# Kernel optimization log

Measured on AMD Instinct MI355X. Metric: run time of the kernel, lower is better.

## Reference

```python
import jax, jax.numpy as jnp
import numpy as np

N = 100000
NFEAT = 128
NHID = 16
HEADS = 8
NCLASS = 40
E = 1600000
NEG_SLOPE = 0.2  # PyG GATConv default


def glorot(key, shape):
    fan = shape[0] + shape[-1]
    limit = float(np.sqrt(6.0 / fan))
    return jax.random.uniform(key, shape, jnp.float32, -limit, limit)


def setup_inputs() -> dict:
    key = jax.random.key(0)
    ks = jax.random.split(key, 10)
    x = jax.random.normal(ks[0], (N, NFEAT), jnp.float32)
    adj = jnp.zeros((1,), jnp.float32)  # unused by forward, kept for signature parity
    edge_index = jax.random.randint(ks[1], (2, E), 0, N, jnp.int64)
    # layer 1: GATConv(NFEAT, NHID, heads=HEADS)
    W1 = glorot(ks[2], (NFEAT, HEADS * NHID))
    att_src1 = glorot(ks[3], (HEADS, NHID))
    att_dst1 = glorot(ks[4], (HEADS, NHID))
    b1 = jnp.zeros((HEADS * NHID,), jnp.float32)
    # layer 2: GATConv(HEADS*NHID, NCLASS, heads=1)
    W2 = glorot(ks[5], (HEADS * NHID, NCLASS))
    att_src2 = glorot(ks[6], (1, NCLASS))
    att_dst2 = glorot(ks[7], (1, NCLASS))
    b2 = jnp.zeros((NCLASS,), jnp.float32)
    return {"x": x, "adj": adj, "edge_index": edge_index,
            "W1": W1, "att_src1": att_src1, "att_dst1": att_dst1, "b1": b1,
            "W2": W2, "att_src2": att_src2, "att_dst2": att_dst2, "b2": b2}


def gat_conv(x, W, att_src, att_dst, bias, src, dst, heads, out_ch):
    n = x.shape[0]
    h = (x @ W).reshape(n, heads, out_ch)              # [N,H,C]
    a_src = (h * att_src[None]).sum(-1)                # [N,H]
    a_dst = (h * att_dst[None]).sum(-1)                # [N,H]
    e = jax.nn.leaky_relu(a_src[src] + a_dst[dst], NEG_SLOPE)  # [E,H]
    # softmax over incoming edges of each destination node
    m = jax.ops.segment_max(e, dst, num_segments=n)
    e = jnp.exp(e - m[dst])
    s = jax.ops.segment_sum(e, dst, num_segments=n)
    alpha = e / s[dst]                                  # [E,H]
    msg = h[src] * alpha[:, :, None]                    # [E,H,C]
    out = jax.ops.segment_sum(msg, dst, num_segments=n)  # [N,H,C]
    return out.reshape(n, heads * out_ch) + bias


def reference(x, adj, edge_index, W1, att_src1, att_dst1, b1, W2, att_src2, att_dst2, b2):
    # PyG GATConv adds self-loops by default
    loops = jnp.arange(N, dtype=edge_index.dtype)
    src = jnp.concatenate([edge_index[0], loops])
    dst = jnp.concatenate([edge_index[1], loops])
    # eval mode: F.dropout is identity
    h = jax.nn.elu(gat_conv(x, W1, att_src1, att_dst1, b1, src, dst, HEADS, NHID))
    h = jax.nn.elu(gat_conv(h, W2, att_src2, att_dst2, b2, src, dst, 1, NCLASS))
    return jax.nn.log_softmax(h, axis=1)
```

## Files before the change

kernel.cpp:

```cpp
#include <hip/hip_runtime.h>
#include <stdint.h>

#define NEG_SLOPE 0.2f

__device__ __forceinline__ float lrelu(float v) { return v >= 0.f ? v : NEG_SLOPE * v; }
__device__ __forceinline__ float elu(float v) { return v > 0.f ? v : expm1f(v); }
__device__ __forceinline__ float pexp(float v) { return __expf(lrelu(v)); }

typedef _Float16 h16x2 __attribute__((ext_vector_type(2)));
typedef _Float16 half8 __attribute__((ext_vector_type(8)));
typedef float floatx4 __attribute__((ext_vector_type(4)));

__device__ __forceinline__ void fma_h2(float& a0, float& a1, float p, unsigned u) {
    h16x2 h = __builtin_bit_cast(h16x2, u);
    a0 += p * (float)h[0];
    a1 += p * (float)h[1];
}


__global__ void prep_kernel(const float* __restrict__ W1, const float* __restrict__ W2,
                            _Float16* __restrict__ w1t, _Float16* __restrict__ w2t,
                            int* __restrict__ deg, int n) {
    int t = blockIdx.x * 256 + threadIdx.x;
    if (t < n) deg[t] = 0;
    if (t < 128 * 128) {
        int col = t >> 7, k = t & 127;
        w1t[col * 128 + k] = (_Float16)W1[k * 128 + col];
    }
    if (t < 48 * 128) {
        int col = t >> 7, k = t & 127;
        w2t[t] = (col < 40) ? (_Float16)W2[k * 40 + col] : (_Float16)0.f;
    }
}


__global__ void hist_kernel(const int* __restrict__ ei, int* __restrict__ deg,
                            unsigned* __restrict__ rankd, int E, int n) {
    int e = blockIdx.x * blockDim.x + threadIdx.x;
    if (e >= E) return;
    int d = ei[E + e];
    unsigned rd = 0xFFFFFFFFu;
    if ((unsigned)d < (unsigned)n)
        rd = ((unsigned)d << 7) | (unsigned)atomicAdd(&deg[d], 1);
    rankd[e] = rd;
}

#define SCAN_T 256
#define SCAN_TILE 1024

__global__ __launch_bounds__(SCAN_T) void scan_p1_kernel(const int* __restrict__ deg,
                                                         int* __restrict__ bsum, int n) {
    __shared__ int red[SCAN_T];
    int t = threadIdx.x;
    int base = blockIdx.x * SCAN_TILE + t * 4;
    int s = 0;
    #pragma unroll
    for (int i = 0; i < 4; i++) {
        int idx = base + i;
        if (idx < n) s += deg[idx];
    }
    red[t] = s;
    __syncthreads();
    for (int off = SCAN_T / 2; off; off >>= 1) {
        if (t < off) red[t] += red[t + off];
        __syncthreads();
    }
    if (t == 0) bsum[blockIdx.x] = red[0];
}

__global__ __launch_bounds__(SCAN_T) void scan_p3f_kernel(const int* __restrict__ deg,
                                                          const int* __restrict__ bsum,
                                                          int* __restrict__ row_ptr,
                                                          int n, int nbk) {
    __shared__ int red[SCAN_T];
    int t = threadIdx.x;
    red[t] = (t < nbk && t < blockIdx.x) ? bsum[t] : 0;
    __syncthreads();
    for (int off = SCAN_T / 2; off; off >>= 1) {
        if (t < off) red[t] += red[t + off];
        __syncthreads();
    }
    const int blockoff = red[0];
    __syncthreads();

    int base = blockIdx.x * SCAN_TILE + t * 4;
    int v[4];
    int s = 0;
    #pragma unroll
    for (int i = 0; i < 4; i++) {
        int idx = base + i;
        v[i] = (idx < n) ? deg[idx] : 0;
        s += v[i];
    }
    red[t] = s;
    __syncthreads();
    for (int off = 1; off < SCAN_T; off <<= 1) {
        int add = (t >= off) ? red[t - off] : 0;
        __syncthreads();
        red[t] += add;
        __syncthreads();
    }
    int excl = red[t] - s + blockoff;
    #pragma unroll
    for (int i = 0; i < 4; i++) {
        int idx = base + i;
        if (idx < n) row_ptr[idx] = excl;
        excl += v[i];
        if (idx == n - 1) row_ptr[n] = excl;
    }
}

__global__ void scatter_kernel(const int* __restrict__ ei, const unsigned* __restrict__ rankd,
                               const int* __restrict__ row_ptr,
                               int* __restrict__ csr_src, int E) {
    int e = blockIdx.x * blockDim.x + threadIdx.x;
    if (e >= E) return;
    unsigned rd = rankd[e];
    if (rd == 0xFFFFFFFFu) return;
    csr_src[row_ptr[rd >> 7] + (int)(rd & 127u)] = ei[e];
}


__global__ __launch_bounds__(256) void gemm1_mfma_kernel(
    const float* __restrict__ x, const _Float16* __restrict__ w1t,
    const float* __restrict__ as1, const float* __restrict__ ad1,
    _Float16* __restrict__ h1h, float* __restrict__ a1s, float* __restrict__ a1d, int n) {
    __shared__ __align__(16) char Wl[32768];
    const int tid = threadIdx.x;
    {
        const uint4* Wg = (const uint4*)w1t;
        #pragma unroll
        for (int i = 0; i < 8; i++) {
            int it = tid + i * 256;
            uint4 v = Wg[it];
            int b = it * 16;
            *(uint4*)&Wl[b ^ (((b >> 8) & 7) << 4)] = v;
        }
    }
    const int wave = tid >> 6, lane = tid & 63;
    const int cl = lane & 15, g = lane >> 4;
    const int wbase = blockIdx.x * 64 + wave * 16;

    int arow = wbase + cl;
    if (arow >= n) arow = n - 1;
    half8 afr[4];
    #pragma unroll
    for (int t = 0; t < 4; t++) {
        const float4 v0 = *(const float4*)&x[(size_t)arow * 128 + 32 * t + g * 8];
        const float4 v1 = *(const float4*)&x[(size_t)arow * 128 + 32 * t + g * 8 + 4];
        afr[t][0] = (_Float16)v0.x; afr[t][1] = (_Float16)v0.y;
        afr[t][2] = (_Float16)v0.z; afr[t][3] = (_Float16)v0.w;
        afr[t][4] = (_Float16)v1.x; afr[t][5] = (_Float16)v1.y;
        afr[t][6] = (_Float16)v1.z; afr[t][7] = (_Float16)v1.w;
    }
    __syncthreads();

    #pragma unroll
    for (int ct = 0; ct < 8; ct++) {
        const int col = ct * 16 + cl;
        half8 bfr[4];
        #pragma unroll
        for (int t = 0; t < 4; t++) {
            int b = (col << 8) + 64 * t + 16 * g;
            bfr[t] = *(half8*)&Wl[b ^ ((col & 7) << 4)];
        }
        floatx4 acc = {0.f, 0.f, 0.f, 0.f};
        #pragma unroll
        for (int t = 0; t < 4; t++)
            acc = __builtin_amdgcn_mfma_f32_16x16x32_f16(afr[t], bfr[t], acc, 0, 0, 0);
        const float av = as1[col], dv = ad1[col];
        #pragma unroll
        for (int i = 0; i < 4; i++) {
            int r = wbase + g * 4 + i;
            float hv = acc[i];
            if (r < n) h1h[(size_t)r * 128 + col] = (_Float16)hv;
            float ps = hv * av, pd = hv * dv;
            ps += __shfl_xor(ps, 1); ps += __shfl_xor(ps, 2);
            ps += __shfl_xor(ps, 4); ps += __shfl_xor(ps, 8);
            pd += __shfl_xor(pd, 1); pd += __shfl_xor(pd, 2);
            pd += __shfl_xor(pd, 4); pd += __shfl_xor(pd, 8);
            if (cl == 0 && r < n) {
                a1s[r * 8 + ct] = ps;
                a1d[r * 8 + ct] = pd;
            }
        }
    }
}

__global__ __launch_bounds__(256) void agg1_kernel(const int* __restrict__ row_ptr,
                                                   const int* __restrict__ csr_src,
                                                   const float* __restrict__ a1s,
                                                   const float* __restrict__ a1d,
                                                   const uint4* __restrict__ h1q,
                                                   const float* __restrict__ b1,
                                                   _Float16* __restrict__ h2h, int n) {
    int lane = threadIdx.x & 63;
    int d = blockIdx.x * 4 + (threadIdx.x >> 6);
    if (d >= n) return;
    const int g = lane >> 4;
    const int q = lane & 15;
    const int h = q >> 1;
    const float adh = a1d[d * 8 + h];

    float acc[8];
    #pragma unroll
    for (int i = 0; i < 8; i++) acc[i] = 0.f;
    float sum = 0.f;
    if (g == 0) {
        uint4 w = h1q[(size_t)d * 16 + q];
        float ps = pexp(a1s[d * 8 + h] + adh);
        fma_h2(acc[0], acc[1], ps, w.x);
        fma_h2(acc[2], acc[3], ps, w.y);
        fma_h2(acc[4], acc[5], ps, w.z);
        fma_h2(acc[6], acc[7], ps, w.w);
        sum = ps;
    }
    int beg = row_ptr[d], end = row_ptr[d + 1];
    int e = beg + g;
    for (; e + 12 < end; e += 16) {
        int s0 = csr_src[e],     s1 = csr_src[e + 4];
        int s2 = csr_src[e + 8], s3 = csr_src[e + 12];
        uint4 w0 = h1q[(size_t)s0 * 16 + q];
        uint4 w1 = h1q[(size_t)s1 * 16 + q];
        uint4 w2 = h1q[(size_t)s2 * 16 + q];
        uint4 w3 = h1q[(size_t)s3 * 16 + q];
        float p0 = pexp(a1s[s0 * 8 + h] + adh);
        float p1 = pexp(a1s[s1 * 8 + h] + adh);
        float p2 = pexp(a1s[s2 * 8 + h] + adh);
        float p3 = pexp(a1s[s3 * 8 + h] + adh);
        fma_h2(acc[0], acc[1], p0, w0.x); fma_h2(acc[2], acc[3], p0, w0.y);
        fma_h2(acc[4], acc[5], p0, w0.z); fma_h2(acc[6], acc[7], p0, w0.w);
        fma_h2(acc[0], acc[1], p1, w1.x); fma_h2(acc[2], acc[3], p1, w1.y);
        fma_h2(acc[4], acc[5], p1, w1.z); fma_h2(acc[6], acc[7], p1, w1.w);
        fma_h2(acc[0], acc[1], p2, w2.x); fma_h2(acc[2], acc[3], p2, w2.y);
        fma_h2(acc[4], acc[5], p2, w2.z); fma_h2(acc[6], acc[7], p2, w2.w);
        fma_h2(acc[0], acc[1], p3, w3.x); fma_h2(acc[2], acc[3], p3, w3.y);
        fma_h2(acc[4], acc[5], p3, w3.z); fma_h2(acc[6], acc[7], p3, w3.w);
        sum += (p0 + p1) + (p2 + p3);
    }
    for (; e + 4 < end; e += 8) {
        int s0 = csr_src[e], s1 = csr_src[e + 4];
        uint4 w0 = h1q[(size_t)s0 * 16 + q];
        uint4 w1 = h1q[(size_t)s1 * 16 + q];
        float p0 = pexp(a1s[s0 * 8 + h] + adh);
        float p1 = pexp(a1s[s1 * 8 + h] + adh);
        fma_h2(acc[0], acc[1], p0, w0.x); fma_h2(acc[2], acc[3], p0, w0.y);
        fma_h2(acc[4], acc[5], p0, w0.z); fma_h2(acc[6], acc[7], p0, w0.w);
        fma_h2(acc[0], acc[1], p1, w1.x); fma_h2(acc[2], acc[3], p1, w1.y);
        fma_h2(acc[4], acc[5], p1, w1.z); fma_h2(acc[6], acc[7], p1, w1.w);
        sum += p0 + p1;
    }
    for (; e < end; e += 4) {
        int s = csr_src[e];
        uint4 w = h1q[(size_t)s * 16 + q];
        float p = pexp(a1s[s * 8 + h] + adh);
        fma_h2(acc[0], acc[1], p, w.x);
        fma_h2(acc[2], acc[3], p, w.y);
        fma_h2(acc[4], acc[5], p, w.z);
        fma_h2(acc[6], acc[7], p, w.w);
        sum += p;
    }
    sum += __shfl_xor(sum, 16); sum += __shfl_xor(sum, 32);
    #pragma unroll
    for (int i = 0; i < 8; i++) {
        acc[i] += __shfl_xor(acc[i], 16);
        acc[i] += __shfl_xor(acc[i], 32);
    }
    if (g == 0) {
        float rs = 1.f / sum;
        float4 b0 = *(const float4*)&b1[8 * q];
        float4 b4 = *(const float4*)&b1[8 * q + 4];
        half8 o;
        o[0] = (_Float16)elu(acc[0] * rs + b0.x);
        o[1] = (_Float16)elu(acc[1] * rs + b0.y);
        o[2] = (_Float16)elu(acc[2] * rs + b0.z);
        o[3] = (_Float16)elu(acc[3] * rs + b0.w);
        o[4] = (_Float16)elu(acc[4] * rs + b4.x);
        o[5] = (_Float16)elu(acc[5] * rs + b4.y);
        o[6] = (_Float16)elu(acc[6] * rs + b4.z);
        o[7] = (_Float16)elu(acc[7] * rs + b4.w);
        *(half8*)&h2h[(size_t)d * 128 + 8 * q] = o;
    }
}


__global__ __launch_bounds__(256) void gemm2_mfma_kernel(
    const _Float16* __restrict__ h2h, const _Float16* __restrict__ w2t,
    const float* __restrict__ as2, const float* __restrict__ ad2,
    _Float16* __restrict__ h3pk, float* __restrict__ a2d, int n) {
    const int tid = threadIdx.x;
    const int wave = tid >> 6, lane = tid & 63;
    const int cl = lane & 15, g = lane >> 4;
    const int wbase = blockIdx.x * 64 + wave * 16;

    int arow = wbase + cl;
    if (arow >= n) arow = n - 1;
    half8 afr[4];
    #pragma unroll
    for (int t = 0; t < 4; t++)
        afr[t] = *(const half8*)&h2h[(size_t)arow * 128 + 32 * t + 8 * g];

    float ps[4] = {0.f, 0.f, 0.f, 0.f};
    float pd[4] = {0.f, 0.f, 0.f, 0.f};
    #pragma unroll
    for (int ct = 0; ct < 3; ct++) {
        const int col = ct * 16 + cl;
        half8 bfr[4];
        #pragma unroll
        for (int t = 0; t < 4; t++)
            bfr[t] = *(const half8*)&w2t[col * 128 + 32 * t + 8 * g];
        floatx4 acc = {0.f, 0.f, 0.f, 0.f};
        #pragma unroll
        for (int t = 0; t < 4; t++)
            acc = __builtin_amdgcn_mfma_f32_16x16x32_f16(afr[t], bfr[t], acc, 0, 0, 0);
        const bool cv = (col < 40);
        const float av = cv ? as2[col] : 0.f;
        const float dv = cv ? ad2[col] : 0.f;
        #pragma unroll
        for (int i = 0; i < 4; i++) {
            int r = wbase + g * 4 + i;
            float hv = acc[i];
            if (cv && r < n)
                h3pk[(size_t)r * 64 + 2 + col] = (_Float16)hv;
            ps[i] += hv * av;
            pd[i] += hv * dv;
        }
    }
    #pragma unroll
    for (int i = 0; i < 4; i++) {
        float s = ps[i], dd = pd[i];
        s += __shfl_xor(s, 1); s += __shfl_xor(s, 2);
        s += __shfl_xor(s, 4); s += __shfl_xor(s, 8);
        dd += __shfl_xor(dd, 1); dd += __shfl_xor(dd, 2);
        dd += __shfl_xor(dd, 4); dd += __shfl_xor(dd, 8);
        int r = wbase + g * 4 + i;
        if (cl == 0 && r < n) {
            ((float*)h3pk)[(size_t)r * 32] = s;
            a2d[r] = dd;
        }
    }
}

__global__ __launch_bounds__(256) void agg2_final_kernel(const int* __restrict__ row_ptr,
                                                         const int* __restrict__ csr_src,
                                                         const unsigned* __restrict__ h3u,
                                                         const float* __restrict__ a2d,
                                                         const float* __restrict__ b2,
                                                         float* __restrict__ out, int n) {
    const float* h3a = (const float*)h3u;
    int lane = threadIdx.x & 63;
    int d = blockIdx.x * 4 + (threadIdx.x >> 6);
    if (d >= n) return;
    const int g = lane >> 5;
    const int q = lane & 31;
    const bool act = (q < 20);
    const float adh = a2d[d];

    h16x2 hsel = {(_Float16)0.f, (_Float16)0.f};
    if (act && g == 0) hsel = __builtin_bit_cast(h16x2, h3u[(size_t)d * 32 + 1 + q]);

    float acc0 = 0.f, acc1 = 0.f, sum = 0.f;
    if (g == 0) {
        float ps = pexp(h3a[(size_t)d * 32] + adh);
        acc0 = ps * (float)hsel[0]; acc1 = ps * (float)hsel[1]; sum = ps;
    }
    int beg = row_ptr[d], end = row_ptr[d + 1];
    int e = beg + g;
    for (; e + 6 < end; e += 8) {
        int s0 = csr_src[e],     s1 = csr_src[e + 2];
        int s2 = csr_src[e + 4], s3 = csr_src[e + 6];
        float a0 = h3a[(size_t)s0 * 32], a1 = h3a[(size_t)s1 * 32];
        float a2 = h3a[(size_t)s2 * 32], a3 = h3a[(size_t)s3 * 32];
        unsigned w0 = 0u, w1 = 0u, w2 = 0u, w3 = 0u;
        if (act) {
            w0 = h3u[(size_t)s0 * 32 + 1 + q]; w1 = h3u[(size_t)s1 * 32 + 1 + q];
            w2 = h3u[(size_t)s2 * 32 + 1 + q]; w3 = h3u[(size_t)s3 * 32 + 1 + q];
        }
        float p0 = pexp(a0 + adh), p1 = pexp(a1 + adh);
        float p2 = pexp(a2 + adh), p3 = pexp(a3 + adh);
        fma_h2(acc0, acc1, p0, w0);
        fma_h2(acc0, acc1, p1, w1);
        fma_h2(acc0, acc1, p2, w2);
        fma_h2(acc0, acc1, p3, w3);
        sum += (p0 + p1) + (p2 + p3);
    }
    for (; e + 2 < end; e += 4) {
        int s0 = csr_src[e], s1 = csr_src[e + 2];
        float a0 = h3a[(size_t)s0 * 32], a1 = h3a[(size_t)s1 * 32];
        unsigned w0 = 0u, w1 = 0u;
        if (act) {
            w0 = h3u[(size_t)s0 * 32 + 1 + q];
            w1 = h3u[(size_t)s1 * 32 + 1 + q];
        }
        float p0 = pexp(a0 + adh), p1 = pexp(a1 + adh);
        fma_h2(acc0, acc1, p0, w0);
        fma_h2(acc0, acc1, p1, w1);
        sum += p0 + p1;
    }
    for (; e < end; e += 2) {
        int s = csr_src[e];
        float pe = pexp(h3a[(size_t)s * 32] + adh);
        unsigned w = act ? h3u[(size_t)s * 32 + 1 + q] : 0u;
        fma_h2(acc0, acc1, pe, w);
        sum += pe;
    }
    sum += __shfl_xor(sum, 32);
    acc0 += __shfl_xor(acc0, 32);
    acc1 += __shfl_xor(acc1, 32);

    float rs = 1.f / sum;
    float v0 = -3.0e38f, v1 = -3.0e38f;
    if (act) {
        v0 = elu(acc0 * rs + b2[2 * q]);
        v1 = elu(acc1 * rs + b2[2 * q + 1]);
    }
    float mx = (act && g == 0) ? fmaxf(v0, v1) : -3.0e38f;
    #pragma unroll
    for (int off = 32; off; off >>= 1) mx = fmaxf(mx, __shfl_xor(mx, off, 64));
    float es = (act && g == 0) ? (__expf(v0 - mx) + __expf(v1 - mx)) : 0.f;
    #pragma unroll
    for (int off = 32; off; off >>= 1) es += __shfl_xor(es, off, 64);
    if (act && g == 0) {
        float ls = logf(es);
        float2 o;
        o.x = v0 - mx - ls;
        o.y = v1 - mx - ls;
        *(float2*)&out[(size_t)d * 40 + 2 * q] = o;
    }
}

extern "C" void kernel_launch(void* const* d_in, const int* in_sizes, int n_in,
                              void* d_out, int out_size, void* d_ws, size_t ws_size,
                              hipStream_t stream) {
    const float* x   = (const float*)d_in[0];
    const int*   ei  = (const int*)d_in[2];
    const float* W1  = (const float*)d_in[3];
    const float* as1 = (const float*)d_in[4];
    const float* ad1 = (const float*)d_in[5];
    const float* b1  = (const float*)d_in[6];
    const float* W2  = (const float*)d_in[7];
    const float* as2 = (const float*)d_in[8];
    const float* ad2 = (const float*)d_in[9];
    const float* b2  = (const float*)d_in[10];
    float* out = (float*)d_out;

    const int n = in_sizes[0] / 128;
    const int E = in_sizes[2] / 2;
    const int nb = (n + SCAN_TILE - 1) / SCAN_TILE;

    float* ws = (float*)d_ws;
    _Float16* h1h = (_Float16*)ws;
    _Float16* h2h = (_Float16*)(ws + (size_t)n * 64);
    float* A  = ws + (size_t)n * 128;
    int* deg    = (int*)A;
    int* bsum   = deg + n;
    float* a1s = A;
    float* a1d = A + (size_t)n * 8;
    float* a2d = A;
    int* row_ptr = (int*)(A + (size_t)n * 16);
    int* csr_src = row_ptr + (n + 1);
    unsigned* rankd = (unsigned*)(csr_src + E);
    _Float16* w1t = (_Float16*)(((uintptr_t)(rankd + E) + 63) & ~(uintptr_t)63);
    _Float16* w2t = w1t + 128 * 128;
    _Float16* h3pk = h1h;

    prep_kernel<<<(n + 255) / 256, 256, 0, stream>>>(W1, W2, w1t, w2t, deg, n);
    hist_kernel<<<(E + 255) / 256, 256, 0, stream>>>(ei, deg, rankd, E, n);
    scan_p1_kernel<<<nb, SCAN_T, 0, stream>>>(deg, bsum, n);
    scan_p3f_kernel<<<nb, SCAN_T, 0, stream>>>(deg, bsum, row_ptr, n, nb);
    scatter_kernel<<<(E + 255) / 256, 256, 0, stream>>>(ei, rankd, row_ptr, csr_src, E);

    gemm1_mfma_kernel<<<(n + 63) / 64, 256, 0, stream>>>(x, w1t, as1, ad1, h1h, a1s, a1d, n);
    agg1_kernel<<<(n + 3) / 4, 256, 0, stream>>>(row_ptr, csr_src, a1s, a1d,
                                                 (const uint4*)h1h, b1, h2h, n);

    gemm2_mfma_kernel<<<(n + 63) / 64, 256, 0, stream>>>(h2h, w2t, as2, ad2, h3pk, a2d, n);
    agg2_final_kernel<<<(n + 3) / 4, 256, 0, stream>>>(row_ptr, csr_src, (const unsigned*)h3pk,
                                                       a2d, b2, out, n);
}
```

Measured before the change: 411.0 us.

## Fuse weight transpose into histogram and partition atomics by destination range

Merges the weight-transpose prep kernel into the degree-histogram kernel and replaces the in-kernel degree zeroing with a memset. Each chunk of edges is now processed by 8 blocks, and each block only performs atomics for destinations in its eighth of the node range. This is meant to localize atomic traffic to a smaller address window, which may help L2/XCD locality on MI355X. The cost is that every edge index is read 8 times and the grid has 8x more blocks.

```diff
diff --git a/kernel.cpp b/kernel.cpp
--- a/kernel.cpp
+++ b/kernel.cpp
@@ -18,32 +18,52 @@
 }
 
 
-__global__ void prep_kernel(const float* __restrict__ W1, const float* __restrict__ W2,
-                            _Float16* __restrict__ w1t, _Float16* __restrict__ w2t,
-                            int* __restrict__ deg, int n) {
-    int t = blockIdx.x * 256 + threadIdx.x;
-    if (t < n) deg[t] = 0;
-    if (t < 128 * 128) {
+#define HC 1024
+
+__global__ __launch_bounds__(256) void hist_wt_kernel(const int* __restrict__ ei,
+                                                      int* __restrict__ deg,
+                                                      unsigned* __restrict__ rankd,
+                                                      const float* __restrict__ W1,
+                                                      const float* __restrict__ W2,
+                                                      _Float16* __restrict__ w1t,
+                                                      _Float16* __restrict__ w2t,
+                                                      int E, int n, int sz) {
+    const int b = blockIdx.x;
+    const int tid = threadIdx.x;
+    if (b < 64) {
+        int t = b * 256 + tid;
         int col = t >> 7, k = t & 127;
         w1t[col * 128 + k] = (_Float16)W1[k * 128 + col];
-    }
-    if (t < 48 * 128) {
-        int col = t >> 7, k = t & 127;
-        w2t[t] = (col < 40) ? (_Float16)W2[k * 40 + col] : (_Float16)0.f;
-    }
-}
-
-
-__global__ void hist_kernel(const int* __restrict__ ei, int* __restrict__ deg,
-                            unsigned* __restrict__ rankd, int E, int n) {
-    int e = blockIdx.x * blockDim.x + threadIdx.x;
-    if (e >= E) return;
-    int d = ei[E + e];
-    unsigned rd = 0xFFFFFFFFu;
-    if ((unsigned)d < (unsigned)n)
-        rd = ((unsigned)d << 7) | (unsigned)atomicAdd(&deg[d], 1);
-    rankd[e] = rd;
-}
+        return;
+    }
+    if (b < 88) {
+        int t = (b - 64) * 256 + tid;
+        if (t < 48 * 128) {
+            int col = t >> 7, k = t & 127;
+            w2t[t] = (col < 40) ? (_Float16)W2[k * 40 + col] : (_Float16)0.f;
+        }
+        return;
+    }
+    const int hb = b - 88;
+    const int c = hb >> 3, r = hb & 7;
+    const int lo = r * sz;
+    const int hi = (lo + sz < n) ? lo + sz : n;
+    const bool last = (r == 7);
+    const int base = c * HC;
+    #pragma unroll
+    for (int i = 0; i < 4; i++) {
+        int e = base + i * 256 + tid;
+        if (e >= E) break;
+        int d = ei[E + e];
+        if (d >= lo && d < hi) {
+            unsigned rk = (unsigned)atomicAdd(&deg[d], 1);
+            rankd[e] = ((unsigned)d << 7) | rk;
+        } else if (last && (unsigned)d >= (unsigned)n) {
+            rankd[e] = 0xFFFFFFFFu;
+        }
+    }
+}
+
 
 #define SCAN_T 256
 #define SCAN_TILE 1024
@@ -447,6 +467,8 @@
     const int n = in_sizes[0] / 128;
     const int E = in_sizes[2] / 2;
     const int nb = (n + SCAN_TILE - 1) / SCAN_TILE;
+    const int nbc = (E + HC - 1) / HC;
+    const int sz = (n + 7) / 8;
 
     float* ws = (float*)d_ws;
     _Float16* h1h = (_Float16*)ws;
@@ -464,8 +486,9 @@
     _Float16* w2t = w1t + 128 * 128;
     _Float16* h3pk = h1h;
 
-    prep_kernel<<<(n + 255) / 256, 256, 0, stream>>>(W1, W2, w1t, w2t, deg, n);
-    hist_kernel<<<(E + 255) / 256, 256, 0, stream>>>(ei, deg, rankd, E, n);
+    hipMemsetAsync(deg, 0, (size_t)n * sizeof(int), stream);
+    hist_wt_kernel<<<88 + nbc * 8, 256, 0, stream>>>(ei, deg, rankd, W1, W2,
+                                                     w1t, w2t, E, n, sz);
     scan_p1_kernel<<<nb, SCAN_T, 0, stream>>>(deg, bsum, n);
     scan_p3f_kernel<<<nb, SCAN_T, 0, stream>>>(deg, bsum, row_ptr, n, nb);
     scatter_kernel<<<(E + 255) / 256, 256, 0, stream>>>(ei, rankd, row_ptr, csr_src, E);
```

Result: no change. 413.3 us (+0.6%).
